# Optimization experiments

Measured on AMD Instinct MI355X. Metric: run time of the kernel, lower is better.

Reference implementation:

```python
import jax, jax.numpy as jnp
import numpy as np

D_MODEL = 1024
NUM_HEADS = 16
HEAD_DIM = D_MODEL // NUM_HEADS  # 64
B, S = 2, 2048


def setup_inputs() -> dict:
    key = jax.random.key(0)
    k1, k2, k3, k4, k5 = jax.random.split(key, 5)
    scale = 1.0 / np.sqrt(D_MODEL)
    return {
        "x": jax.random.normal(k1, (B, S, D_MODEL), dtype=jnp.float32),
        "Wq": jax.random.normal(k2, (D_MODEL, D_MODEL), dtype=jnp.float32) * scale,
        "bq": jax.random.normal(k3, (D_MODEL,), dtype=jnp.float32) * 0.02,
        "Wv": jax.random.normal(k4, (D_MODEL, D_MODEL), dtype=jnp.float32) * scale,
        "bv": jax.random.normal(k5, (D_MODEL,), dtype=jnp.float32) * 0.02,
    }


def reference(x, Wq, bq, Wv, bv):
    b, s, _ = x.shape
    d, n = HEAD_DIM, NUM_HEADS
    # nn.Linear: y = x @ W.T + b
    Q = x @ Wq.T + bq
    # NOTE (faithful to source bug): K uses the VALUE projection, key weights unused.
    KV = x @ Wv.T + bv
    # einops 'B S (d n) -> B S d n' -> 'B n S d'  (head index n is fast-varying)
    Qh = Q.reshape(b, s, d, n).transpose(0, 3, 1, 2)   # [B, n, S, d]
    Kt = KV.reshape(b, s, d, n).transpose(0, 3, 2, 1)  # [B, n, d, S]
    Vh = KV.reshape(b, s, d, n).transpose(0, 3, 1, 2)  # [B, n, S, d]
    scores = jnp.matmul(Qh, Kt) / jnp.sqrt(jnp.float32(d))  # [B, n, S, S]
    attn = jnp.matmul(jax.nn.softmax(scores, axis=-1), Vh)  # [B, n, S, d]
    # 'B n S d -> B S (n d)'
    out = attn.transpose(0, 2, 1, 3).reshape(b, s, n * d)
    return out
```

## Files before the change

kernel.cpp:

```cpp
#include <hip/hip_runtime.h>
#include <hip/hip_bf16.h>
#include <math.h>


typedef __bf16 bf16x8 __attribute__((ext_vector_type(8)));
typedef float  f32x4  __attribute__((ext_vector_type(4)));
typedef short  s16x4  __attribute__((ext_vector_type(4)));
typedef unsigned short ushort_t;
typedef unsigned short us8 __attribute__((ext_vector_type(8)));

#define QSCALE 0.1803368801111204f

__device__ __forceinline__ unsigned short f2bf(float f) {
  unsigned int u = __builtin_bit_cast(unsigned int, f);
  u += 0x7fffu + ((u >> 16) & 1u);
  return (unsigned short)(u >> 16);
}

__device__ __forceinline__ unsigned int pk2(float a, float b) {
  unsigned int ua = __builtin_bit_cast(unsigned int, a) + 0x8000u;
  unsigned int ub = __builtin_bit_cast(unsigned int, b) + 0x8000u;
  return (ua >> 16) | (ub & 0xffff0000u);
}

__device__ __forceinline__ void gl_lds16(const void* g, void* l) {
  __builtin_amdgcn_global_load_lds(
      (const __attribute__((address_space(1))) unsigned int*)g,
      (__attribute__((address_space(3))) unsigned int*)l, 16, 0, 0);
}

__device__ __forceinline__ f32x4 mfma_k32(bf16x8 a, bf16x8 b, f32x4 c) {
  return __builtin_amdgcn_mfma_f32_16x16x32_bf16(a, b, c, 0, 0, 0);
}
__device__ __forceinline__ f32x4 mfma_k16(s16x4 a, s16x4 b, f32x4 c) {
  return __builtin_amdgcn_mfma_f32_16x16x16bf16_1k(a, b, c, 0, 0, 0);
}

__global__ __launch_bounds__(256) void cvt3_kernel(const float4* __restrict__ x,
                                                   const float4* __restrict__ wq,
                                                   const float4* __restrict__ wv,
                                                   ushort4* __restrict__ dst) {
  const int i = blockIdx.x * 256 + threadIdx.x;
  const float4 v = (i < 1048576) ? x[i]
                 : (i < 1310720) ? wq[i - 1048576]
                                 : wv[i - 1310720];
  ushort4 o;
  o.x = f2bf(v.x); o.y = f2bf(v.y); o.z = f2bf(v.z); o.w = f2bf(v.w);
  dst[i] = o;
}

__global__ __launch_bounds__(256) void proj_kernel(
    const ushort_t* __restrict__ X,
    const ushort_t* __restrict__ Wqm,
    const ushort_t* __restrict__ Wvm,
    const float*    __restrict__ bq,
    const float*    __restrict__ bv,
    ushort_t* __restrict__ Qh,
    ushort_t* __restrict__ KVh,
    ushort_t* __restrict__ KVt)
{
  __shared__ __align__(16) unsigned char lds[32768];
  const int tid = threadIdx.x;
  const int w  = tid >> 6;
  const int l  = tid & 63;
  const int lq = l >> 4;
  const int ll = l & 15;
  const bool isQ = (blockIdx.z == 0);
  const ushort_t* Wmat = isQ ? Wqm : Wvm;
  const float*    bias = isQ ? bq  : bv;
  const int m0 = blockIdx.x * 128;
  const int by = blockIdx.y;
  const int wm = (w & 1) * 64;
  const int wn = (w >> 1) * 64;

  f32x4 acc[4][4] = {};

  for (int k0 = 0; k0 < 1024; k0 += 64) {
    __syncthreads();
#pragma unroll
    for (int t = 0; t < 4; ++t) {
      const int seg = w * 4 + t;
      const int r = seg * 8 + (l >> 3);
      const int cd = (l & 7) ^ (r & 7);
      const int cg = by * 128 + r;
      const int wrow = ((cg & 63) << 4) | (cg >> 6);
      gl_lds16(X    + (size_t)(m0 + r) * 1024 + k0 + cd * 8, lds + seg * 1024);
      gl_lds16(Wmat + (size_t)wrow * 1024 + k0 + cd * 8, lds + 16384 + seg * 1024);
    }
    __syncthreads();
#pragma unroll
    for (int kb = 0; kb < 2; ++kb) {
      const int kc = kb * 4 + lq;
      bf16x8 af[4], bfr[4];
#pragma unroll
      for (int mi = 0; mi < 4; ++mi) {
        const int m = wm + mi * 16 + ll;
        af[mi] = *(const bf16x8*)(lds + m * 128 + ((kc ^ (m & 7)) * 16));
      }
#pragma unroll
      for (int ni = 0; ni < 4; ++ni) {
        const int n = wn + ni * 16 + ll;
        bfr[ni] = *(const bf16x8*)(lds + 16384 + n * 128 + ((kc ^ (n & 7)) * 16));
      }
#pragma unroll
      for (int mi = 0; mi < 4; ++mi)
#pragma unroll
        for (int ni = 0; ni < 4; ++ni)
          acc[mi][ni] = mfma_k32(af[mi], bfr[ni], acc[mi][ni]);
    }
  }

  const int hl = wn >> 6;
  const int hh = by * 2 + hl;
  const int b  = m0 >> 11;
  const int sbase = m0 & 2047;

  if (isQ) {
#pragma unroll
    for (int ni = 0; ni < 4; ++ni) {
      const int ii = ni * 16 + ll;
      const float bb = bias[(ii << 4) | hh];
#pragma unroll
      for (int mi = 0; mi < 4; ++mi)
#pragma unroll
        for (int r = 0; r < 4; ++r) {
          const int s = sbase + wm + mi * 16 + lq * 4 + r;
          const float v = acc[mi][ni][r] + bb;
          Qh[(((size_t)(b * 16 + hh)) * 2048 + s) * 64 + ii] = f2bf(v * QSCALE);
        }
    }
  } else {
    __syncthreads();
#pragma unroll
    for (int ni = 0; ni < 4; ++ni) {
      const int ii = ni * 16 + ll;
      const float bb = bias[(ii << 4) | hh];
#pragma unroll
      for (int mi = 0; mi < 4; ++mi) {
        const float v0 = acc[mi][ni][0] + bb;
        const float v1 = acc[mi][ni][1] + bb;
        const float v2 = acc[mi][ni][2] + bb;
        const float v3 = acc[mi][ni][3] + bb;
        const unsigned int u01 = pk2(v0, v1);
        const unsigned int u23 = pk2(v2, v3);
        const int sl = wm + mi * 16 + lq * 4;
        const size_t kb0 = (((size_t)(b * 16 + hh)) * 2048 + sbase + sl) * 64 + ii;
        KVh[kb0]       = (ushort_t)(u01 & 0xffffu);
        KVh[kb0 + 64]  = (ushort_t)(u01 >> 16);
        KVh[kb0 + 128] = (ushort_t)(u23 & 0xffffu);
        KVh[kb0 + 192] = (ushort_t)(u23 >> 16);
        const int g = (wm >> 2) + mi * 4 + lq;
        const int pc = (g >> 1) ^ ll;
        *(uint2*)(lds + hl * 16384 + ii * 256 + pc * 16 + (g & 1) * 8) =
            make_uint2(u01, u23);
      }
    }
    __syncthreads();
    const int row = tid >> 1;
    const int hl2 = row >> 6, ii2 = row & 63;
    const int cbase = (tid & 1) * 8;
    ushort_t* dst = KVt + (((size_t)(b * 16 + by * 2 + hl2)) * 64 + ii2) * 2048 + sbase;
#pragma unroll
    for (int cc = 0; cc < 8; ++cc) {
      const int c = cbase + cc;
      const int pc = c ^ (ii2 & 15);
      const us8 v = *(const us8*)(lds + hl2 * 16384 + ii2 * 256 + pc * 16);
      *(us8*)(dst + c * 8) = v;
    }
  }
}

__global__ __launch_bounds__(256, 4) void attn_kernel(
    const ushort_t* __restrict__ Qh,
    const ushort_t* __restrict__ KVh,
    const ushort_t* __restrict__ KVt,
    float* __restrict__ out)
{
  __shared__ __align__(16) unsigned char sm[32768];
  const int tid = threadIdx.x;
  const int w  = tid >> 6;
  const int l  = tid & 63;
  const int quad = l >> 4;
  const int ll = l & 15;
  const int bid = blockIdx.x;
  const int bh = ((bid & 7) << 2) | (bid >> 8);
  const int qt = (bid >> 3) & 31;
  const int b = bh >> 4, h = bh & 15;
  const int qw = qt * 64 + w * 16;
  const ushort_t* Qhead  = Qh  + (size_t)bh * (2048 * 64);
  const ushort_t* Khead  = KVh + (size_t)bh * (2048 * 64);
  const ushort_t* Vthead = KVt + (size_t)bh * (64 * 2048);

  bf16x8 qf[2];
#pragma unroll
  for (int kb = 0; kb < 2; ++kb)
    qf[kb] = *(const bf16x8*)(Qhead + (size_t)(qw + ll) * 64 + kb * 32 + quad * 8);

  f32x4 O[4] = {};
  float l_run = 0.f;

  for (int kt = 0; kt < 16; ++kt) {
    const int sk0 = kt * 128;
    __syncthreads();
#pragma unroll
    for (int t = 0; t < 4; ++t) {
      const int seg = w * 4 + t;
      const int r = seg * 8 + (l >> 3);
      const int cd = (l & 7) ^ (r & 7);
      gl_lds16(Khead + (size_t)(sk0 + r) * 64 + cd * 8, sm + seg * 1024);
    }
#pragma unroll
    for (int t = 0; t < 4; ++t) {
      const int seg = w * 4 + t;
      const int d = seg * 4 + (l >> 4);
      const int c8 = (l & 15) ^ (d & 15);
      gl_lds16(Vthead + (size_t)d * 2048 + sk0 + c8 * 8, sm + 16384 + seg * 1024);
    }
    __syncthreads();

    f32x4 Sa[8] = {};
#pragma unroll
    for (int kb = 0; kb < 2; ++kb) {
      const int kc = kb * 4 + quad;
#pragma unroll
      for (int ni = 0; ni < 8; ++ni) {
        const int n = ni * 16 + ll;
        const bf16x8 ak = *(const bf16x8*)(sm + n * 128 + ((kc ^ (n & 7)) * 16));
        Sa[ni] = mfma_k32(ak, qf[kb], Sa[ni]);
      }
    }

    float ps = 0.f;
    s16x4 pk[8];
#pragma unroll
    for (int ni = 0; ni < 8; ++ni) {
      const float p0 = __builtin_amdgcn_exp2f(Sa[ni][0]);
      const float p1 = __builtin_amdgcn_exp2f(Sa[ni][1]);
      const float p2 = __builtin_amdgcn_exp2f(Sa[ni][2]);
      const float p3 = __builtin_amdgcn_exp2f(Sa[ni][3]);
      ps += (p0 + p1) + (p2 + p3);
      const uint2 uu = make_uint2(pk2(p0, p1), pk2(p2, p3));
      pk[ni] = __builtin_bit_cast(s16x4, uu);
    }
    ps += __shfl_xor(ps, 16);
    ps += __shfl_xor(ps, 32);
    l_run += ps;

#pragma unroll
    for (int ni = 0; ni < 8; ++ni) {
      const int cb = 2 * ni + (quad >> 1);
#pragma unroll
      for (int no = 0; no < 4; ++no) {
        const int row = no * 16 + ll;
        const s16x4 bv = *(const s16x4*)(sm + 16384 + row * 256 +
                                         ((cb ^ ll) * 16) + (quad & 1) * 8);
        O[no] = mfma_k16(pk[ni], bv, O[no]);
      }
    }
  }

  const float inv = 1.f / l_run;
  float invr[4];
#pragma unroll
  for (int r = 0; r < 4; ++r)
    invr[r] = __shfl(inv, (l & 48) + ((l & 48) >> 2) + r);

  float* op = out + ((size_t)(b * 2048) + qw) * 1024 + h * 64;
#pragma unroll
  for (int no = 0; no < 4; ++no)
#pragma unroll
    for (int r = 0; r < 4; ++r) {
      const int q = quad * 4 + r;
      op[(size_t)q * 1024 + no * 16 + ll] = O[no][r] * invr[r];
    }
}

extern "C" void kernel_launch(void* const* d_in, const int* in_sizes, int n_in,
                              void* d_out, int out_size, void* d_ws, size_t ws_size,
                              hipStream_t stream) {
  const float* x  = (const float*)d_in[0];
  const float* Wq = (const float*)d_in[1];
  const float* bq = (const float*)d_in[2];
  const float* Wv = (const float*)d_in[3];
  const float* bv = (const float*)d_in[4];
  float* out = (float*)d_out;
  char* ws = (char*)d_ws;

  ushort_t* xbf  = (ushort_t*)(ws);
  ushort_t* wqbf = (ushort_t*)(ws + 8388608);
  ushort_t* wvbf = (ushort_t*)(ws + 10485760);
  ushort_t* Qh   = (ushort_t*)(ws + 12582912);
  ushort_t* KVh  = (ushort_t*)(ws + 20971520);
  ushort_t* KVt  = (ushort_t*)(ws + 29360128);

  cvt3_kernel<<<6144, 256, 0, stream>>>((const float4*)x, (const float4*)Wq,
                                        (const float4*)Wv, (ushort4*)xbf);
  proj_kernel<<<dim3(32, 8, 2), 256, 0, stream>>>(xbf, wqbf, wvbf, bq, bv,
                                                  Qh, KVh, KVt);
  attn_kernel<<<1024, 256, 0, stream>>>(Qh, KVh, KVt, out);
}
```

Baseline: 157.7 us.

## Process two query sub-tiles per wave in attention to reuse K/V LDS fragments

Halves the attention block to 128 threads (2 waves) while each wave now handles 32 query rows as two 16-row sub-tiles. Each K and V fragment read from LDS feeds two MFMAs, which halves LDS read traffic per MFMA. The cost is more accumulator registers per wave, fewer waves per block to hide latency, and each wave issuing twice as many global-to-LDS loads per tile. The launch bound minimum occupancy drops from 4 to 2.

New measurement: 156.6 us. No clear change (-0.7%).

```diff
diff --git a/kernel.cpp b/kernel.cpp
--- a/kernel.cpp
+++ b/kernel.cpp
@@ -170,7 +170,7 @@
   }
 }
 
-__global__ __launch_bounds__(256, 4) void attn_kernel(
+__global__ __launch_bounds__(128, 2) void attn_kernel(
     const ushort_t* __restrict__ Qh,
     const ushort_t* __restrict__ KVh,
     const ushort_t* __restrict__ KVt,
@@ -186,39 +186,42 @@
   const int bh = ((bid & 7) << 2) | (bid >> 8);
   const int qt = (bid >> 3) & 31;
   const int b = bh >> 4, h = bh & 15;
-  const int qw = qt * 64 + w * 16;
+  const int qw = qt * 64 + w * 32;
   const ushort_t* Qhead  = Qh  + (size_t)bh * (2048 * 64);
   const ushort_t* Khead  = KVh + (size_t)bh * (2048 * 64);
   const ushort_t* Vthead = KVt + (size_t)bh * (64 * 2048);
 
-  bf16x8 qf[2];
-#pragma unroll
-  for (int kb = 0; kb < 2; ++kb)
-    qf[kb] = *(const bf16x8*)(Qhead + (size_t)(qw + ll) * 64 + kb * 32 + quad * 8);
-
-  f32x4 O[4] = {};
-  float l_run = 0.f;
+  bf16x8 qf[2][2];
+#pragma unroll
+  for (int c = 0; c < 2; ++c)
+#pragma unroll
+    for (int kb = 0; kb < 2; ++kb)
+      qf[c][kb] = *(const bf16x8*)(Qhead + (size_t)(qw + c * 16 + ll) * 64 +
+                                   kb * 32 + quad * 8);
+
+  f32x4 O[2][4] = {};
+  float l_run[2] = {0.f, 0.f};
 
   for (int kt = 0; kt < 16; ++kt) {
     const int sk0 = kt * 128;
     __syncthreads();
 #pragma unroll
-    for (int t = 0; t < 4; ++t) {
-      const int seg = w * 4 + t;
+    for (int t = 0; t < 8; ++t) {
+      const int seg = w * 8 + t;
       const int r = seg * 8 + (l >> 3);
       const int cd = (l & 7) ^ (r & 7);
       gl_lds16(Khead + (size_t)(sk0 + r) * 64 + cd * 8, sm + seg * 1024);
     }
 #pragma unroll
-    for (int t = 0; t < 4; ++t) {
-      const int seg = w * 4 + t;
+    for (int t = 0; t < 8; ++t) {
+      const int seg = w * 8 + t;
       const int d = seg * 4 + (l >> 4);
       const int c8 = (l & 15) ^ (d & 15);
       gl_lds16(Vthead + (size_t)d * 2048 + sk0 + c8 * 8, sm + 16384 + seg * 1024);
     }
     __syncthreads();
 
-    f32x4 Sa[8] = {};
+    f32x4 Sa[2][8] = {};
 #pragma unroll
     for (int kb = 0; kb < 2; ++kb) {
       const int kc = kb * 4 + quad;
@@ -226,25 +229,29 @@
       for (int ni = 0; ni < 8; ++ni) {
         const int n = ni * 16 + ll;
         const bf16x8 ak = *(const bf16x8*)(sm + n * 128 + ((kc ^ (n & 7)) * 16));
-        Sa[ni] = mfma_k32(ak, qf[kb], Sa[ni]);
-      }
-    }
-
-    float ps = 0.f;
-    s16x4 pk[8];
-#pragma unroll
-    for (int ni = 0; ni < 8; ++ni) {
-      const float p0 = __builtin_amdgcn_exp2f(Sa[ni][0]);
-      const float p1 = __builtin_amdgcn_exp2f(Sa[ni][1]);
-      const float p2 = __builtin_amdgcn_exp2f(Sa[ni][2]);
-      const float p3 = __builtin_amdgcn_exp2f(Sa[ni][3]);
-      ps += (p0 + p1) + (p2 + p3);
-      const uint2 uu = make_uint2(pk2(p0, p1), pk2(p2, p3));
-      pk[ni] = __builtin_bit_cast(s16x4, uu);
-    }
-    ps += __shfl_xor(ps, 16);
-    ps += __shfl_xor(ps, 32);
-    l_run += ps;
+        Sa[0][ni] = mfma_k32(ak, qf[0][kb], Sa[0][ni]);
+        Sa[1][ni] = mfma_k32(ak, qf[1][kb], Sa[1][ni]);
+      }
+    }
+
+    s16x4 pk[2][8];
+#pragma unroll
+    for (int c = 0; c < 2; ++c) {
+      float ps = 0.f;
+#pragma unroll
+      for (int ni = 0; ni < 8; ++ni) {
+        const float p0 = __builtin_amdgcn_exp2f(Sa[c][ni][0]);
+        const float p1 = __builtin_amdgcn_exp2f(Sa[c][ni][1]);
+        const float p2 = __builtin_amdgcn_exp2f(Sa[c][ni][2]);
+        const float p3 = __builtin_amdgcn_exp2f(Sa[c][ni][3]);
+        ps += (p0 + p1) + (p2 + p3);
+        const uint2 uu = make_uint2(pk2(p0, p1), pk2(p2, p3));
+        pk[c][ni] = __builtin_bit_cast(s16x4, uu);
+      }
+      ps += __shfl_xor(ps, 16);
+      ps += __shfl_xor(ps, 32);
+      l_run[c] += ps;
+    }
 
 #pragma unroll
     for (int ni = 0; ni < 8; ++ni) {
@@ -254,25 +261,28 @@
         const int row = no * 16 + ll;
         const s16x4 bv = *(const s16x4*)(sm + 16384 + row * 256 +
                                          ((cb ^ ll) * 16) + (quad & 1) * 8);
-        O[no] = mfma_k16(pk[ni], bv, O[no]);
+        O[0][no] = mfma_k16(pk[0][ni], bv, O[0][no]);
+        O[1][no] = mfma_k16(pk[1][ni], bv, O[1][no]);
       }
     }
   }
 
-  const float inv = 1.f / l_run;
-  float invr[4];
-#pragma unroll
-  for (int r = 0; r < 4; ++r)
-    invr[r] = __shfl(inv, (l & 48) + ((l & 48) >> 2) + r);
-
-  float* op = out + ((size_t)(b * 2048) + qw) * 1024 + h * 64;
-#pragma unroll
-  for (int no = 0; no < 4; ++no)
-#pragma unroll
-    for (int r = 0; r < 4; ++r) {
-      const int q = quad * 4 + r;
-      op[(size_t)q * 1024 + no * 16 + ll] = O[no][r] * invr[r];
-    }
+#pragma unroll
+  for (int c = 0; c < 2; ++c) {
+    const float inv = 1.f / l_run[c];
+    float invr[4];
+#pragma unroll
+    for (int r = 0; r < 4; ++r)
+      invr[r] = __shfl(inv, (l & 48) + ((l & 48) >> 2) + r);
+    float* op = out + ((size_t)(b * 2048) + qw + c * 16) * 1024 + h * 64;
+#pragma unroll
+    for (int no = 0; no < 4; ++no)
+#pragma unroll
+      for (int r = 0; r < 4; ++r) {
+        const int q = quad * 4 + r;
+        op[(size_t)q * 1024 + no * 16 + ll] = O[c][no][r] * invr[r];
+      }
+  }
 }
 
 extern "C" void kernel_launch(void* const* d_in, const int* in_sizes, int n_in,
@@ -297,5 +307,5 @@
                                         (const float4*)Wv, (ushort4*)xbf);
   proj_kernel<<<dim3(32, 8, 2), 256, 0, stream>>>(xbf, wqbf, wvbf, bq, bv,
                                                   Qh, KVh, KVt);
-  attn_kernel<<<1024, 256, 0, stream>>>(Qh, KVh, KVt, out);
-}
+  attn_kernel<<<1024, 128, 0, stream>>>(Qh, KVh, KVt, out);
+}
```
